# Kernel tuning notes

Measured on AMD Instinct MI355X. Metric: run time of the kernel, lower is better.

## Reference

```python
import jax, jax.numpy as jnp
import numpy as np

IN_FEATURES = 4096
OUT_FEATURES = 4096
N_TOKENS = 8192  # flattened batch*seq


def setup_inputs() -> dict:
    key = jax.random.key(0)
    kx, kw = jax.random.split(key)
    x = jax.random.normal(kx, (N_TOKENS, IN_FEATURES), dtype=jnp.float16)
    # Full weight [out, in], split into a 2:4 structured part and the complement
    # (mirrors prune_2_to_4's [0,0,1,1] pattern along the in dim).
    W = jax.random.normal(kw, (OUT_FEATURES, IN_FEATURES), dtype=jnp.float16)
    pattern = jnp.asarray([0, 0, 1, 1], dtype=jnp.float16)
    mask = jnp.tile(pattern, IN_FEATURES // 4)  # [in]
    W_dense = W * mask          # 2:4 semi-structured component
    W_sparse = W * (1 - mask)   # unstructured CSR component (complement)
    return {"x": x, "W_dense": W_dense, "W_sparse": W_sparse}


def reference(x, W_dense, W_sparse):
    # Original: out_dense = W_semi @ x^T ; out_sparse = spmm(W_csr, x^T)
    #           out = out_sparse^T + out_dense^T
    # Equivalent: x @ W_dense^T + x @ W_sparse^T, two separate GEMMs summed.
    out_dense = jnp.einsum('ni,oi->no', x, W_dense)
    out_sparse = jnp.einsum('ni,oi->no', x, W_sparse)
    return out_dense + out_sparse
```

## Files before the change

### kernel.cpp

```cpp
#include <hip/hip_runtime.h>
#include <stdint.h>


#define NT 8192
#define NO 4096
#define NK 4096

typedef float f32x4 __attribute__((ext_vector_type(4)));
typedef _Float16 f16x8 __attribute__((ext_vector_type(8)));
typedef __bf16 bf16x8 __attribute__((ext_vector_type(8)));
typedef short short8 __attribute__((ext_vector_type(8)));

__device__ __forceinline__ void gload_lds16(const void* g, void* l) {
  __builtin_amdgcn_global_load_lds(
      (const __attribute__((address_space(1))) void*)g,
      (__attribute__((address_space(3))) void*)l, 16, 0, 0);
}

#define BAR() __builtin_amdgcn_s_barrier()
#define WV6() asm volatile("s_waitcnt vmcnt(6)" ::: "memory")
#define PRIO1() __builtin_amdgcn_s_setprio(1)
#define PRIO0() __builtin_amdgcn_s_setprio(0)

__device__ __forceinline__ short f32_bf16(float f) {
  uint32_t u = __float_as_uint(f);
  u += 0x7FFFu + ((u >> 16) & 1u);
  return (short)(u >> 16);
}

__global__ __launch_bounds__(256) void cvt_all(
    const float* __restrict__ x, const float* __restrict__ wd,
    const float* __restrict__ ws, short* __restrict__ xh,
    short* __restrict__ wh, int nx8, int nw8) {
  int i = blockIdx.x * 256 + threadIdx.x;
  if (i < nx8) {
    const f32x4* p = (const f32x4*)x + 2 * (size_t)i;
    f32x4 lo = p[0], hi = p[1];
    short8 r;
#pragma unroll
    for (int j = 0; j < 4; ++j) { r[j] = f32_bf16(lo[j]); r[j + 4] = f32_bf16(hi[j]); }
    *((short8*)xh + i) = r;
  } else {
    int j8 = i - nx8;
    if (j8 < nw8) {
      const f32x4* pd = (const f32x4*)wd + 2 * (size_t)j8;
      const f32x4* ps = (const f32x4*)ws + 2 * (size_t)j8;
      f32x4 dl = pd[0], dh = pd[1], sl = ps[0], sh = ps[1];
      short8 r;
#pragma unroll
      for (int j = 0; j < 4; ++j) {
        r[j] = f32_bf16(dl[j] + sl[j]);
        r[j + 4] = f32_bf16(dh[j] + sh[j]);
      }
      *((short8*)wh + j8) = r;
    }
  }
}


#define RDA(B_, MG) do { _Pragma("unroll") \
  for (int mm = 0; mm < 4; ++mm) { \
    ar[0][mm] = *(const short8*)(Ab[B_] + ((MG)*8 + mm*2 + 0) * 1024 + finner); \
    ar[1][mm] = *(const short8*)(Ab[B_] + ((MG)*8 + mm*2 + 1) * 1024 + finner); \
  } } while (0)

#define RDB(B_, NG) do { _Pragma("unroll") \
  for (int nn = 0; nn < 2; ++nn) { \
    br[0][(NG)*2+nn] = *(const short8*)(Bb[B_] + ((bsub + (NG)*2 + nn)*2 + 0) * 1024 + finner); \
    br[1][(NG)*2+nn] = *(const short8*)(Bb[B_] + ((bsub + (NG)*2 + nn)*2 + 1) * 1024 + finner); \
  } } while (0)

#define MM(MG, NG) do { _Pragma("unroll") \
  for (int ks = 0; ks < 2; ++ks) \
    _Pragma("unroll") for (int mm = 0; mm < 4; ++mm) \
      _Pragma("unroll") for (int nn = 0; nn < 2; ++nn) \
        acc[(MG)*4+mm][(NG)*2+nn] = __builtin_amdgcn_mfma_f32_16x16x32_bf16( \
            __builtin_bit_cast(bf16x8, br[ks][(NG)*2+nn]), \
            __builtin_bit_cast(bf16x8, ar[ks][mm]), \
            acc[(MG)*4+mm][(NG)*2+nn], 0, 0, 0); \
  } while (0)

#define STG(BUF_, OP_, H_, S_, KCOL) \
  gload_lds16(((OP_) ? Wrow : Xrow) + ((H_)*128 + (S_)*64) * NK + (KCOL), \
              ldsc + (BUF_)*65536 + (OP_)*32768 + (H_)*16384 + (S_)*8192 + t16)

__global__ __launch_bounds__(512, 2) void gemm8p(
    const short* __restrict__ Xg, const short* __restrict__ Wg,
    float* __restrict__ C) {
  __shared__ short lds[2][2][2][8192];
  char* ldsc = (char*)&lds[0][0][0][0];

  const int t = threadIdx.x;
  const int lane = t & 63;
  const int wv = t >> 6;
  const int wr = wv >> 2;
  const int wc = wv & 3;
  const int fr = lane & 15;
  const int kq = lane >> 4;
  const int t16 = t * 16;

  const int swz = (blockIdx.x & 7) * 64 + (blockIdx.x >> 3);
  const int bm = swz >> 4, bn = swz & 15;
  const int brow = bm * 256, bcol = bn * 256;

  const int o = t16;
  const int sub = o >> 10;
  const int inner = o & 1023;
  const int innsw = inner ^ (((inner >> 9) & 1) << 5);
  const int rloc = ((sub >> 1) << 4) | ((innsw >> 6) & 15);
  const int kloc = ((sub & 1) << 5) | ((innsw >> 1) & 31);

  const short* Xrow = Xg + (brow + rloc) * NK + kloc;
  const short* Wrow = Wg + (bcol + rloc) * NK + kloc;

  const int finner = ((fr << 6) | (kq << 4)) ^ ((fr & 8) << 2);
  const char* Ab[2] = { ldsc + wr * 16384, ldsc + 65536 + wr * 16384 };
  const char* Bb[2] = { ldsc + 32768 + (wc >> 1) * 16384,
                        ldsc + 65536 + 32768 + (wc >> 1) * 16384 };
  const int bsub = (wc & 1) * 4;

  short8 ar[2][4], br[2][4];
  f32x4 acc[8][4] = {};

  STG(0, 0, 0, 0, 0); STG(0, 0, 0, 1, 0); STG(0, 0, 1, 0, 0); STG(0, 0, 1, 1, 0);
  STG(0, 1, 0, 0, 0); STG(0, 1, 0, 1, 0); STG(0, 1, 1, 0, 0); STG(0, 1, 1, 1, 0);
  STG(1, 0, 0, 0, 64); STG(1, 0, 1, 0, 64);
  STG(1, 1, 0, 0, 64); STG(1, 1, 0, 1, 64); STG(1, 1, 1, 0, 64); STG(1, 1, 1, 1, 64);
  WV6(); BAR();

#pragma unroll 1
  for (int i = 0; i < NK / 128; ++i) {
    const int k1 = i * 128 + 64;
    const int kt2 = (i * 128 + 128) & (NK - 1);
    const int kt3 = (i * 128 + 192) & (NK - 1);

    RDA(0, 0); RDB(0, 0);
    STG(1, 0, 0, 1, k1); STG(1, 0, 1, 1, k1);
    PRIO1(); MM(0, 0); PRIO0(); BAR();
    RDB(0, 1);
    STG(0, 0, 0, 0, kt2); STG(0, 0, 1, 0, kt2);
    PRIO1(); MM(0, 1); PRIO0(); BAR();
    RDA(0, 1);
    STG(0, 1, 0, 0, kt2); STG(0, 1, 0, 1, kt2);
    PRIO1(); MM(1, 0); PRIO0(); BAR();
    STG(0, 1, 1, 0, kt2); STG(0, 1, 1, 1, kt2);
    PRIO1(); MM(1, 1); PRIO0();
    WV6(); BAR();
    RDA(1, 0); RDB(1, 0);
    STG(0, 0, 0, 1, kt2); STG(0, 0, 1, 1, kt2);
    PRIO1(); MM(0, 0); PRIO0(); BAR();
    RDB(1, 1);
    STG(1, 0, 0, 0, kt3); STG(1, 0, 1, 0, kt3);
    PRIO1(); MM(0, 1); PRIO0(); BAR();
    RDA(1, 1);
    STG(1, 1, 0, 0, kt3); STG(1, 1, 0, 1, kt3);
    PRIO1(); MM(1, 0); PRIO0(); BAR();
    STG(1, 1, 1, 0, kt3); STG(1, 1, 1, 1, kt3);
    PRIO1(); MM(1, 1); PRIO0();
    WV6(); BAR();
  }

  const long r0 = brow + wr * 128 + fr;
  const int c0 = bcol + wc * 64 + kq * 4;
#pragma unroll
  for (int m = 0; m < 8; ++m)
#pragma unroll
    for (int n = 0; n < 4; ++n)
      *(f32x4*)(C + (r0 + m * 16) * NO + c0 + n * 16) = acc[m][n];
}

__global__ __launch_bounds__(256) void gemm_fb(
    const float* __restrict__ Xf, const float* __restrict__ Wdf,
    const float* __restrict__ Wsf, float* __restrict__ C) {
  __shared__ _Float16 lsA[128 * 32];
  __shared__ _Float16 lsB[128 * 32];

  const int t = threadIdx.x;
  const int lane = t & 63;
  const int wid = t >> 6;
  const int wr = wid >> 1, wc = wid & 1;

  const int nwg = (NT / 128) * (NO / 128);
  const int swz = (blockIdx.x & 7) * (nwg >> 3) + (blockIdx.x >> 3);
  const int nbn = NO / 128;
  const int bm = swz / nbn, bn = swz % nbn;
  const long brow = (long)bm * 128, bcol = (long)bn * 128;

  const int srow = t >> 2;
  const int scol = (t & 3) * 8;
  const float* X  = Xf + (brow + srow) * (long)NK + scol;
  const float* Wd = Wdf + (bcol + srow) * (long)NK + scol;
  const float* Ws = Wsf + (bcol + srow) * (long)NK + scol;
  _Float16* lA = lsA + t * 8;
  _Float16* lB = lsB + t * 8;

  const int fr = lane & 15;
  const int kg = (lane >> 4) * 8;
  const _Float16* pA = lsA + (wr * 64 + fr) * 32 + kg;
  const _Float16* pB = lsB + (wc * 64 + fr) * 32 + kg;

  f32x4 acc[4][4] = {};

  for (int k0 = 0; k0 < NK; k0 += 32) {
    f32x4 aL0 = *(const f32x4*)(X + k0),  aH0 = *(const f32x4*)(X + k0 + 4);
    f32x4 aL1 = *(const f32x4*)(X + k0 + 64 * NK), aH1 = *(const f32x4*)(X + k0 + 64 * NK + 4);
    f32x4 dL0 = *(const f32x4*)(Wd + k0), dH0 = *(const f32x4*)(Wd + k0 + 4);
    f32x4 sL0 = *(const f32x4*)(Ws + k0), sH0 = *(const f32x4*)(Ws + k0 + 4);
    f32x4 dL1 = *(const f32x4*)(Wd + k0 + 64 * NK), dH1 = *(const f32x4*)(Wd + k0 + 64 * NK + 4);
    f32x4 sL1 = *(const f32x4*)(Ws + k0 + 64 * NK), sH1 = *(const f32x4*)(Ws + k0 + 64 * NK + 4);
    __syncthreads();
    f16x8 va0, va1, vb0, vb1;
#pragma unroll
    for (int j = 0; j < 4; ++j) {
      va0[j] = (_Float16)aL0[j];            va0[j + 4] = (_Float16)aH0[j];
      va1[j] = (_Float16)aL1[j];            va1[j + 4] = (_Float16)aH1[j];
      vb0[j] = (_Float16)(dL0[j] + sL0[j]); vb0[j + 4] = (_Float16)(dH0[j] + sH0[j]);
      vb1[j] = (_Float16)(dL1[j] + sL1[j]); vb1[j + 4] = (_Float16)(dH1[j] + sH1[j]);
    }
    *(f16x8*)lA = va0;
    *(f16x8*)(lA + 64 * 32) = va1;
    *(f16x8*)lB = vb0;
    *(f16x8*)(lB + 64 * 32) = vb1;
    __syncthreads();
    f16x8 af[4], bf[4];
#pragma unroll
    for (int i2 = 0; i2 < 4; ++i2) af[i2] = *(const f16x8*)(pA + i2 * 16 * 32);
#pragma unroll
    for (int i2 = 0; i2 < 4; ++i2) bf[i2] = *(const f16x8*)(pB + i2 * 16 * 32);
#pragma unroll
    for (int i2 = 0; i2 < 4; ++i2)
#pragma unroll
      for (int j2 = 0; j2 < 4; ++j2)
        acc[i2][j2] = __builtin_amdgcn_mfma_f32_16x16x32_f16(af[i2], bf[j2], acc[i2][j2], 0, 0, 0);
  }

  const int fq = lane >> 4;
#pragma unroll
  for (int i2 = 0; i2 < 4; ++i2)
#pragma unroll
    for (int j2 = 0; j2 < 4; ++j2)
#pragma unroll
      for (int r = 0; r < 4; ++r) {
        long row = brow + wr * 64 + i2 * 16 + fq * 4 + r;
        long col = bcol + wc * 64 + j2 * 16 + fr;
        C[row * NO + col] = acc[i2][j2][r];
      }
}

extern "C" void kernel_launch(void* const* d_in, const int* in_sizes, int n_in,
                              void* d_out, int out_size, void* d_ws, size_t ws_size,
                              hipStream_t stream) {
  const float* x   = (const float*)d_in[0];
  const float* wd  = (const float*)d_in[1];
  const float* wsp = (const float*)d_in[2];
  float* out = (float*)d_out;

  const size_t xh_bytes = (size_t)NT * NK * 2;
  const size_t wh_bytes = (size_t)NO * NK * 2;

  if (d_ws != nullptr && ws_size >= xh_bytes + wh_bytes) {
    short* xh = (short*)d_ws;
    short* wh = (short*)((char*)d_ws + xh_bytes);
    const int nx8 = NT * NK / 8;
    const int nw8 = NO * NK / 8;
    cvt_all<<<(nx8 + nw8) / 256, 256, 0, stream>>>(x, wd, wsp, xh, wh, nx8, nw8);
    gemm8p<<<(NT / 256) * (NO / 256), 512, 0, stream>>>(xh, wh, out);
  } else {
    gemm_fb<<<(NT / 128) * (NO / 128), 256, 0, stream>>>(x, wd, wsp, out);
  }
}
```

Baseline: 285.9 us.

## Replace 256x256 GEMM with 128x256 tile triple-buffered high-occupancy kernel

```diff
diff --git a/kernel.cpp b/kernel.cpp
--- a/kernel.cpp
+++ b/kernel.cpp
@@ -18,7 +18,8 @@
 }
 
 #define BAR() __builtin_amdgcn_s_barrier()
-#define WV6() asm volatile("s_waitcnt vmcnt(6)" ::: "memory")
+#define WV3() asm volatile("s_waitcnt vmcnt(3)" ::: "memory")
+#define WV0() asm volatile("s_waitcnt vmcnt(0)" ::: "memory")
 #define PRIO1() __builtin_amdgcn_s_setprio(1)
 #define PRIO0() __builtin_amdgcn_s_setprio(0)
 
@@ -58,37 +59,33 @@
 }
 
 
-#define RDA(B_, MG) do { _Pragma("unroll") \
-  for (int mm = 0; mm < 4; ++mm) { \
-    ar[0][mm] = *(const short8*)(Ab[B_] + ((MG)*8 + mm*2 + 0) * 1024 + finner); \
-    ar[1][mm] = *(const short8*)(Ab[B_] + ((MG)*8 + mm*2 + 1) * 1024 + finner); \
-  } } while (0)
-
-#define RDB(B_, NG) do { _Pragma("unroll") \
-  for (int nn = 0; nn < 2; ++nn) { \
-    br[0][(NG)*2+nn] = *(const short8*)(Bb[B_] + ((bsub + (NG)*2 + nn)*2 + 0) * 1024 + finner); \
-    br[1][(NG)*2+nn] = *(const short8*)(Bb[B_] + ((bsub + (NG)*2 + nn)*2 + 1) * 1024 + finner); \
-  } } while (0)
-
-#define MM(MG, NG) do { _Pragma("unroll") \
-  for (int ks = 0; ks < 2; ++ks) \
-    _Pragma("unroll") for (int mm = 0; mm < 4; ++mm) \
-      _Pragma("unroll") for (int nn = 0; nn < 2; ++nn) \
-        acc[(MG)*4+mm][(NG)*2+nn] = __builtin_amdgcn_mfma_f32_16x16x32_bf16( \
-            __builtin_bit_cast(bf16x8, br[ks][(NG)*2+nn]), \
-            __builtin_bit_cast(bf16x8, ar[ks][mm]), \
-            acc[(MG)*4+mm][(NG)*2+nn], 0, 0, 0); \
-  } while (0)
-
-#define STG(BUF_, OP_, H_, S_, KCOL) \
-  gload_lds16(((OP_) ? Wrow : Xrow) + ((H_)*128 + (S_)*64) * NK + (KCOL), \
-              ldsc + (BUF_)*65536 + (OP_)*32768 + (H_)*16384 + (S_)*8192 + t16)
-
-__global__ __launch_bounds__(512, 2) void gemm8p(
+#define RD_OCC(BUF_) do { \
+  const char* Ab_ = ldsc + (BUF_) * 24576 + aoff; \
+  const char* Bb_ = ldsc + (BUF_) * 24576 + boff; \
+  br[0] = *(const short8*)(Bb_ + 0);    ar[0] = *(const short8*)(Ab_ + 0); \
+  br[1] = *(const short8*)(Bb_ + 1024); br[2] = *(const short8*)(Bb_ + 2048); \
+  br[3] = *(const short8*)(Bb_ + 3072); ar[1] = *(const short8*)(Ab_ + 1024); \
+  ar[2] = *(const short8*)(Ab_ + 2048); ar[3] = *(const short8*)(Ab_ + 3072); \
+} while (0)
+
+#define STG_OCC(BUF_, KCOL) do { \
+  gload_lds16(Xrow + (KCOL), ldsc + (BUF_) * 24576 + t16); \
+  gload_lds16(Wrow + (KCOL), ldsc + (BUF_) * 24576 + 8192 + t16); \
+  gload_lds16(Wrow + 128 * NK + (KCOL), ldsc + (BUF_) * 24576 + 16384 + t16); \
+} while (0)
+
+#define MM_OCC() do { PRIO1(); _Pragma("unroll") \
+  for (int m = 0; m < 4; ++m) _Pragma("unroll") for (int n = 0; n < 4; ++n) \
+    acc[m][n] = __builtin_amdgcn_mfma_f32_16x16x32_bf16( \
+        __builtin_bit_cast(bf16x8, br[n]), __builtin_bit_cast(bf16x8, ar[m]), \
+        acc[m][n], 0, 0, 0); \
+  PRIO0(); } while (0)
+
+__global__ __launch_bounds__(512, 4) void gemm_occ(
     const short* __restrict__ Xg, const short* __restrict__ Wg,
     float* __restrict__ C) {
-  __shared__ short lds[2][2][2][8192];
-  char* ldsc = (char*)&lds[0][0][0][0];
+  __shared__ short lds[3][12288];
+  char* ldsc = (char*)&lds[0][0];
 
   const int t = threadIdx.x;
   const int lane = t & 63;
@@ -99,71 +96,48 @@
   const int kq = lane >> 4;
   const int t16 = t * 16;
 
-  const int swz = (blockIdx.x & 7) * 64 + (blockIdx.x >> 3);
+  const int swz = (blockIdx.x & 7) * 128 + (blockIdx.x >> 3);
   const int bm = swz >> 4, bn = swz & 15;
-  const int brow = bm * 256, bcol = bn * 256;
+  const int brow = bm * 128, bcol = bn * 256;
 
   const int o = t16;
   const int sub = o >> 10;
   const int inner = o & 1023;
   const int innsw = inner ^ (((inner >> 9) & 1) << 5);
-  const int rloc = ((sub >> 1) << 4) | ((innsw >> 6) & 15);
-  const int kloc = ((sub & 1) << 5) | ((innsw >> 1) & 31);
+  const int rloc = sub * 16 + ((innsw >> 6) & 15);
+  const int kloc = (innsw >> 1) & 31;
 
   const short* Xrow = Xg + (brow + rloc) * NK + kloc;
   const short* Wrow = Wg + (bcol + rloc) * NK + kloc;
 
   const int finner = ((fr << 6) | (kq << 4)) ^ ((fr & 8) << 2);
-  const char* Ab[2] = { ldsc + wr * 16384, ldsc + 65536 + wr * 16384 };
-  const char* Bb[2] = { ldsc + 32768 + (wc >> 1) * 16384,
-                        ldsc + 65536 + 32768 + (wc >> 1) * 16384 };
-  const int bsub = (wc & 1) * 4;
-
-  short8 ar[2][4], br[2][4];
-  f32x4 acc[8][4] = {};
-
-  STG(0, 0, 0, 0, 0); STG(0, 0, 0, 1, 0); STG(0, 0, 1, 0, 0); STG(0, 0, 1, 1, 0);
-  STG(0, 1, 0, 0, 0); STG(0, 1, 0, 1, 0); STG(0, 1, 1, 0, 0); STG(0, 1, 1, 1, 0);
-  STG(1, 0, 0, 0, 64); STG(1, 0, 1, 0, 64);
-  STG(1, 1, 0, 0, 64); STG(1, 1, 0, 1, 64); STG(1, 1, 1, 0, 64); STG(1, 1, 1, 1, 64);
-  WV6(); BAR();
+  const int aoff = wr * 4096 + finner;
+  const int boff = 8192 + (wc >> 1) * 8192 + (wc & 1) * 4096 + finner;
+
+  short8 ar[4], br[4];
+  f32x4 acc[4][4] = {};
+
+  STG_OCC(0, 0);
+  STG_OCC(1, 32);
+  WV3(); BAR();
 
 #pragma unroll 1
-  for (int i = 0; i < NK / 128; ++i) {
-    const int k1 = i * 128 + 64;
-    const int kt2 = (i * 128 + 128) & (NK - 1);
-    const int kt3 = (i * 128 + 192) & (NK - 1);
-
-    RDA(0, 0); RDB(0, 0);
-    STG(1, 0, 0, 1, k1); STG(1, 0, 1, 1, k1);
-    PRIO1(); MM(0, 0); PRIO0(); BAR();
-    RDB(0, 1);
-    STG(0, 0, 0, 0, kt2); STG(0, 0, 1, 0, kt2);
-    PRIO1(); MM(0, 1); PRIO0(); BAR();
-    RDA(0, 1);
-    STG(0, 1, 0, 0, kt2); STG(0, 1, 0, 1, kt2);
-    PRIO1(); MM(1, 0); PRIO0(); BAR();
-    STG(0, 1, 1, 0, kt2); STG(0, 1, 1, 1, kt2);
-    PRIO1(); MM(1, 1); PRIO0();
-    WV6(); BAR();
-    RDA(1, 0); RDB(1, 0);
-    STG(0, 0, 0, 1, kt2); STG(0, 0, 1, 1, kt2);
-    PRIO1(); MM(0, 0); PRIO0(); BAR();
-    RDB(1, 1);
-    STG(1, 0, 0, 0, kt3); STG(1, 0, 1, 0, kt3);
-    PRIO1(); MM(0, 1); PRIO0(); BAR();
-    RDA(1, 1);
-    STG(1, 1, 0, 0, kt3); STG(1, 1, 0, 1, kt3);
-    PRIO1(); MM(1, 0); PRIO0(); BAR();
-    STG(1, 1, 1, 0, kt3); STG(1, 1, 1, 1, kt3);
-    PRIO1(); MM(1, 1); PRIO0();
-    WV6(); BAR();
-  }
-
-  const long r0 = brow + wr * 128 + fr;
+  for (int i = 0; i < 42; ++i) {
+    const int kc = i * 96;
+    RD_OCC(0); STG_OCC(2, kc + 64);
+    MM_OCC(); WV3(); BAR();
+    RD_OCC(1); STG_OCC(0, kc + 96);
+    MM_OCC(); WV3(); BAR();
+    RD_OCC(2); STG_OCC(1, kc + 128);
+    MM_OCC(); WV3(); BAR();
+  }
+  RD_OCC(0); MM_OCC(); WV0(); BAR();
+  RD_OCC(1); MM_OCC();
+
+  const long r0 = brow + wr * 64 + fr;
   const int c0 = bcol + wc * 64 + kq * 4;
 #pragma unroll
-  for (int m = 0; m < 8; ++m)
+  for (int m = 0; m < 4; ++m)
 #pragma unroll
     for (int n = 0; n < 4; ++n)
       *(f32x4*)(C + (r0 + m * 16) * NO + c0 + n * 16) = acc[m][n];
@@ -264,7 +238,7 @@
     const int nx8 = NT * NK / 8;
     const int nw8 = NO * NK / 8;
     cvt_all<<<(nx8 + nw8) / 256, 256, 0, stream>>>(x, wd, wsp, xh, wh, nx8, nw8);
-    gemm8p<<<(NT / 256) * (NO / 256), 512, 0, stream>>>(xh, wh, out);
+    gemm_occ<<<(NT / 128) * (NO / 256), 512, 0, stream>>>(xh, wh, out);
   } else {
     gemm_fb<<<(NT / 128) * (NO / 128), 256, 0, stream>>>(x, wd, wsp, out);
   }
```

New measurement: 354.6 us. 1.24x slower.

## Load A operand directly from global into registers, stage only B in LDS

Applied to the files above, without the earlier changes.

```diff
diff --git a/kernel.cpp b/kernel.cpp
--- a/kernel.cpp
+++ b/kernel.cpp
@@ -18,7 +18,9 @@
 }
 
 #define BAR() __builtin_amdgcn_s_barrier()
-#define WV6() asm volatile("s_waitcnt vmcnt(6)" ::: "memory")
+#define WV28() asm volatile("s_waitcnt vmcnt(28)" ::: "memory")
+#define WV12() asm volatile("s_waitcnt vmcnt(12)" ::: "memory")
+#define WV0() asm volatile("s_waitcnt vmcnt(0)" ::: "memory")
 #define PRIO1() __builtin_amdgcn_s_setprio(1)
 #define PRIO0() __builtin_amdgcn_s_setprio(0)
 
@@ -58,19 +60,19 @@
 }
 
 
-#define RDA(B_, MG) do { _Pragma("unroll") \
+#define GLA(MG_, KT_) do { _Pragma("unroll") \
   for (int mm = 0; mm < 4; ++mm) { \
-    ar[0][mm] = *(const short8*)(Ab[B_] + ((MG)*8 + mm*2 + 0) * 1024 + finner); \
-    ar[1][mm] = *(const short8*)(Ab[B_] + ((MG)*8 + mm*2 + 1) * 1024 + finner); \
+    ar[0][mm] = *(const short8*)(Arow + ((MG_)*64 + mm*16) * (long)NK + (KT_)); \
+    ar[1][mm] = *(const short8*)(Arow + ((MG_)*64 + mm*16) * (long)NK + (KT_) + 32); \
   } } while (0)
 
-#define RDB(B_, NG) do { _Pragma("unroll") \
+#define LDB(B_, NG) do { _Pragma("unroll") \
   for (int nn = 0; nn < 2; ++nn) { \
     br[0][(NG)*2+nn] = *(const short8*)(Bb[B_] + ((bsub + (NG)*2 + nn)*2 + 0) * 1024 + finner); \
     br[1][(NG)*2+nn] = *(const short8*)(Bb[B_] + ((bsub + (NG)*2 + nn)*2 + 1) * 1024 + finner); \
   } } while (0)
 
-#define MM(MG, NG) do { _Pragma("unroll") \
+#define MM(MG, NG) do { PRIO1(); _Pragma("unroll") \
   for (int ks = 0; ks < 2; ++ks) \
     _Pragma("unroll") for (int mm = 0; mm < 4; ++mm) \
       _Pragma("unroll") for (int nn = 0; nn < 2; ++nn) \
@@ -78,17 +80,17 @@
             __builtin_bit_cast(bf16x8, br[ks][(NG)*2+nn]), \
             __builtin_bit_cast(bf16x8, ar[ks][mm]), \
             acc[(MG)*4+mm][(NG)*2+nn], 0, 0, 0); \
-  } while (0)
-
-#define STG(BUF_, OP_, H_, S_, KCOL) \
-  gload_lds16(((OP_) ? Wrow : Xrow) + ((H_)*128 + (S_)*64) * NK + (KCOL), \
-              ldsc + (BUF_)*65536 + (OP_)*32768 + (H_)*16384 + (S_)*8192 + t16)
+  PRIO0(); } while (0)
+
+#define STGB(BUF_, H_, S_, KCOL) \
+  gload_lds16(Wrow + ((H_)*128 + (S_)*64) * NK + (KCOL), \
+              ldsc + (BUF_)*32768 + (H_)*16384 + (S_)*8192 + t16)
 
 __global__ __launch_bounds__(512, 2) void gemm8p(
     const short* __restrict__ Xg, const short* __restrict__ Wg,
     float* __restrict__ C) {
-  __shared__ short lds[2][2][2][8192];
-  char* ldsc = (char*)&lds[0][0][0][0];
+  __shared__ short lds[2][2][8192];
+  char* ldsc = (char*)&lds[0][0][0];
 
   const int t = threadIdx.x;
   const int lane = t & 63;
@@ -109,55 +111,66 @@
   const int innsw = inner ^ (((inner >> 9) & 1) << 5);
   const int rloc = ((sub >> 1) << 4) | ((innsw >> 6) & 15);
   const int kloc = ((sub & 1) << 5) | ((innsw >> 1) & 31);
-
-  const short* Xrow = Xg + (brow + rloc) * NK + kloc;
   const short* Wrow = Wg + (bcol + rloc) * NK + kloc;
 
+  const short* Arow = Xg + (brow + wr * 128 + fr) * (long)NK + kq * 8;
+
   const int finner = ((fr << 6) | (kq << 4)) ^ ((fr & 8) << 2);
-  const char* Ab[2] = { ldsc + wr * 16384, ldsc + 65536 + wr * 16384 };
-  const char* Bb[2] = { ldsc + 32768 + (wc >> 1) * 16384,
-                        ldsc + 65536 + 32768 + (wc >> 1) * 16384 };
+  const char* Bb[2] = { ldsc + (wc >> 1) * 16384,
+                        ldsc + 32768 + (wc >> 1) * 16384 };
   const int bsub = (wc & 1) * 4;
 
   short8 ar[2][4], br[2][4];
   f32x4 acc[8][4] = {};
 
-  STG(0, 0, 0, 0, 0); STG(0, 0, 0, 1, 0); STG(0, 0, 1, 0, 0); STG(0, 0, 1, 1, 0);
-  STG(0, 1, 0, 0, 0); STG(0, 1, 0, 1, 0); STG(0, 1, 1, 0, 0); STG(0, 1, 1, 1, 0);
-  STG(1, 0, 0, 0, 64); STG(1, 0, 1, 0, 64);
-  STG(1, 1, 0, 0, 64); STG(1, 1, 0, 1, 64); STG(1, 1, 1, 0, 64); STG(1, 1, 1, 1, 64);
-  WV6(); BAR();
+  STGB(0, 0, 0, 0); STGB(0, 0, 1, 0); STGB(0, 1, 0, 0); STGB(0, 1, 1, 0);
+  STGB(1, 0, 0, 64); STGB(1, 0, 1, 64); STGB(1, 1, 0, 64); STGB(1, 1, 1, 64);
+  GLA(0, 0);
+  WV12(); BAR();
 
 #pragma unroll 1
-  for (int i = 0; i < NK / 128; ++i) {
-    const int k1 = i * 128 + 64;
-    const int kt2 = (i * 128 + 128) & (NK - 1);
-    const int kt3 = (i * 128 + 192) & (NK - 1);
-
-    RDA(0, 0); RDB(0, 0);
-    STG(1, 0, 0, 1, k1); STG(1, 0, 1, 1, k1);
-    PRIO1(); MM(0, 0); PRIO0(); BAR();
-    RDB(0, 1);
-    STG(0, 0, 0, 0, kt2); STG(0, 0, 1, 0, kt2);
-    PRIO1(); MM(0, 1); PRIO0(); BAR();
-    RDA(0, 1);
-    STG(0, 1, 0, 0, kt2); STG(0, 1, 0, 1, kt2);
-    PRIO1(); MM(1, 0); PRIO0(); BAR();
-    STG(0, 1, 1, 0, kt2); STG(0, 1, 1, 1, kt2);
-    PRIO1(); MM(1, 1); PRIO0();
-    WV6(); BAR();
-    RDA(1, 0); RDB(1, 0);
-    STG(0, 0, 0, 1, kt2); STG(0, 0, 1, 1, kt2);
-    PRIO1(); MM(0, 0); PRIO0(); BAR();
-    RDB(1, 1);
-    STG(1, 0, 0, 0, kt3); STG(1, 0, 1, 0, kt3);
-    PRIO1(); MM(0, 1); PRIO0(); BAR();
-    RDA(1, 1);
-    STG(1, 1, 0, 0, kt3); STG(1, 1, 0, 1, kt3);
-    PRIO1(); MM(1, 0); PRIO0(); BAR();
-    STG(1, 1, 1, 0, kt3); STG(1, 1, 1, 1, kt3);
-    PRIO1(); MM(1, 1); PRIO0();
-    WV6(); BAR();
+  for (int i = 0; i < NK / 128 - 1; ++i) {
+    const int kc = i * 128;
+    const int kt2 = kc + 128;
+    const int kt3 = kc + 192;
+
+    LDB(0, 0);
+    MM(0, 0); BAR();
+    LDB(0, 1);
+    MM(0, 1);
+    GLA(1, kc);
+    BAR();
+    STGB(0, 0, 0, kt2); STGB(0, 0, 1, kt2);
+    MM(1, 0); BAR();
+    STGB(0, 1, 0, kt2); STGB(0, 1, 1, kt2);
+    MM(1, 1);
+    GLA(0, kc + 64);
+    WV28(); BAR();
+    LDB(1, 0);
+    MM(0, 0); BAR();
+    LDB(1, 1);
+    MM(0, 1);
+    GLA(1, kc + 64);
+    BAR();
+    STGB(1, 0, 0, kt3); STGB(1, 0, 1, kt3);
+    MM(1, 0); BAR();
+    STGB(1, 1, 0, kt3); STGB(1, 1, 1, kt3);
+    MM(1, 1);
+    GLA(0, kt2);
+    WV28(); BAR();
+  }
+
+  {
+    const int kc = (NK / 128 - 1) * 128;
+    LDB(0, 0); MM(0, 0); BAR();
+    LDB(0, 1); MM(0, 1); GLA(1, kc); BAR();
+    MM(1, 0); BAR();
+    MM(1, 1); GLA(0, kc + 64);
+    WV0(); BAR();
+    LDB(1, 0); MM(0, 0); BAR();
+    LDB(1, 1); MM(0, 1); GLA(1, kc + 64); BAR();
+    MM(1, 0); BAR();
+    MM(1, 1);
   }
 
   const long r0 = brow + wr * 128 + fr;
```

Measured after the change: 734.2 us. 157% more time.
